# Kernel tuning notes

Measured on AMD Instinct MI355X. Metric: run time of the kernel, lower is better.

Reference implementation:

```python
import jax, jax.numpy as jnp
import numpy as np

NEG_INF = float('-inf')
B, T, C, U = 32, 1000, 500, 100
RISK_FACTOR = 0.1  # risk_strategy='exp', group_strategy='end'


def _lse3(x1, x2, x3):
    # numerically-safe logsumexp of 3 args, nan-free grads at -inf
    m = jnp.maximum(jnp.maximum(x1, x2), x3)
    dead = jnp.isneginf(m)
    ms = jnp.where(dead, 0.0, m)
    s = jnp.exp(x1 - ms) + jnp.exp(x2 - ms) + jnp.exp(x3 - ms)
    s = jnp.where(dead, 1.0, s)
    return jnp.where(dead, NEG_INF, ms + jnp.log(s))


def _safe_lse(x, axis):
    m = jnp.max(x, axis=axis, keepdims=True)
    dead = jnp.isneginf(m)
    ms = jnp.where(dead, 0.0, m)
    s = jnp.sum(jnp.exp(x - ms), axis=axis, keepdims=True)
    s = jnp.where(dead, 1.0, s)
    out = jnp.where(dead, NEG_INF, ms + jnp.log(s))
    return jnp.squeeze(out, axis)


def _log_sub_exp(a, b):
    # faithful port of espnet's log_substraction_exp: log(exp(a)-exp(b))
    mask1 = (~jnp.isinf(a)) & (~jnp.isinf(b))
    a_ = jnp.where(mask1, a, -1.0)
    b_ = jnp.where(mask1, b, -2.0)
    ans_tmp = b_ + jnp.log(jnp.exp(a_ - b_) - 1.0)
    a2 = jnp.where(jnp.isinf(ans_tmp), -2000.0, a_)
    b2 = jnp.where(jnp.isinf(ans_tmp), -2001.0, b_)
    ans1 = b2 + jnp.log(jnp.exp(a2 - b2) - 1.0)
    ans = jnp.where(mask1, ans1, jnp.full_like(a, NEG_INF))
    mask2 = (~jnp.isinf(a)) & jnp.isinf(b)
    return jnp.where(mask2, a, ans)


def _shift_r(x, n):
    return jnp.pad(x[:, :-n], ((0, 0), (n, 0)), constant_values=NEG_INF)


def _shift_l(x, n):
    return jnp.pad(x[:, n:], ((0, 0), (0, n)), constant_values=NEG_INF)


def _brctc_loss(nnet_output, ys_pad, hlens, ylens):
    # Dense equivalent of the k2 CTC lattice forward-backward in the log semiring.
    Bb, Tt, Cc = nnet_output.shape
    Uu = ys_pad.shape[1]
    S = 2 * Uu + 1  # extended label states: blank,y1,blank,...,yU,blank
    dt = nnet_output.dtype
    s_idx = jnp.arange(S)
    lab = ys_pad[:, jnp.clip((s_idx - 1) // 2, 0, Uu - 1)]        # [B,S]
    labels_ext = jnp.where((s_idx % 2 == 1)[None, :], lab, 0)
    prev_lab = ys_pad[:, jnp.clip((s_idx - 3) // 2, 0, Uu - 1)]
    allow_skip = ((s_idx % 2 == 1) & (s_idx >= 3))[None, :] & (lab != prev_lab)
    # p_ext[b,t,s] = nnet_output[b,t,labels_ext[b,s]]
    p_ext = jnp.take_along_axis(
        nnet_output, jnp.broadcast_to(labels_ext[:, None, :], (Bb, Tt, S)), axis=2)
    valid_s = s_idx[None, :] <= 2 * ylens[:, None]                # states beyond 2*ylen don't exist
    p_ext = jnp.where(valid_s[:, None, :], p_ext, NEG_INF)
    p_tbs = jnp.transpose(p_ext, (1, 0, 2))                       # [T,B,S]

    # forward: alpha[t,s] includes emission at frame t
    def fstep(a, pt):
        anew = pt + _lse3(a, _shift_r(a, 1),
                          jnp.where(allow_skip, _shift_r(a, 2), NEG_INF))
        return anew, anew
    a0 = jnp.full((Bb, S), NEG_INF, dt).at[:, 0].set(0.0)  # virtual start state
    _, alpha = jax.lax.scan(fstep, a0, p_tbs)                     # [T,B,S]

    # backward: beta[t,s] covers frames t+1..hlen-1 (excludes emission at t)
    t_arr = jnp.arange(Tt)
    fin = (s_idx[None, :] == 2 * ylens[:, None]) | (s_idx[None, :] == 2 * ylens[:, None] - 1)
    beta_fin = jnp.where(fin, 0.0, NEG_INF).astype(dt)
    allow_skip_n2 = jnp.pad(allow_skip[:, 2:], ((0, 0), (0, 2)), constant_values=False)
    p_next = jnp.concatenate([p_tbs[1:], jnp.full((1, Bb, S), NEG_INF, dt)], axis=0)

    def bstep(bcarry, inp):
        t, pn = inp
        q = pn + bcarry
        cand = _lse3(q, _shift_l(q, 1),
                     jnp.where(allow_skip_n2, _shift_l(q, 2), NEG_INF))
        bnew = jnp.where((t == hlens - 1)[:, None], beta_fin, cand)
        return bnew, bnew
    _, beta = jax.lax.scan(bstep, jnp.full((Bb, S), NEG_INF, dt),
                           (t_arr, p_next), reverse=True)         # [T,B,S]

    alpha = jnp.transpose(alpha, (1, 2, 0))                       # [B,S,T]
    beta = jnp.transpose(beta, (1, 2, 0))
    alpha = jnp.where((t_arr[None, :] < hlens[:, None])[:, None, :], alpha, NEG_INF)

    # keep only label (odd) states, as in alpha[:, 1::2]
    a_l = alpha[:, 1::2, :]
    b_l = beta[:, 1::2, :]
    p_l = jnp.transpose(p_ext, (0, 2, 1))[:, 1::2, :]
    dead = jnp.isneginf(a_l)  # states absent from the lattice
    b_l = jnp.where(dead, NEG_INF, b_l)
    p_l = jnp.where(dead, NEG_INF, p_l)

    # beta' removes the self-loop continuation -> posterior of label u ending at t
    beta_prime = _log_sub_exp(b_l[:, :, :-1], b_l[:, :, 1:] + p_l[:, :, 1:])
    beta_prime = jnp.concatenate([beta_prime, b_l[:, :, -1:]], axis=-1)
    loss_state = a_l + beta_prime                                 # [B,U,T]

    # risk_strategy == 'exp': risk = -risk_factor * t / hlen
    risk = -RISK_FACTOR * (t_arr[None, None, :].astype(dt) / hlens[:, None, None].astype(dt))
    loss_state = loss_state + risk

    loss_u = _safe_lse(loss_state, 2)                             # [B,U]
    mask = ~jnp.isneginf(loss_u)
    last = jnp.sum(mask.astype(jnp.int32), axis=1) - 1            # = ylen-1
    loss = jnp.take_along_axis(loss_u, last[:, None], axis=1)[:, 0]
    return -loss


def setup_inputs():
    key = jax.random.key(0)
    k1, k2, k3, k4 = jax.random.split(key, 4)
    nnet_output = jax.nn.log_softmax(
        jax.random.normal(k1, (B, T, C), dtype=jnp.float32), axis=-1)
    ys_pad = jax.random.randint(k2, (B, U), 1, C, dtype=jnp.int32)  # labels, 0 = blank excluded
    ylens = jax.random.randint(k3, (B,), 80, U + 1, dtype=jnp.int32)
    hlens = jax.random.randint(k4, (B,), 800, T + 1, dtype=jnp.int32)
    return {'nnet_output': nnet_output, 'ys_pad': ys_pad, 'hlens': hlens, 'ylens': ylens}


def reference(nnet_output, ys_pad, hlens, ylens):
    return _brctc_loss(nnet_output, ys_pad, hlens, ylens)
```

## Files before the change

### kernel.cpp

```cpp
#include <hip/hip_runtime.h>
#include <math.h>

#define T_DIM 1000
#define C_DIM 500
#define U_DIM 100
#define PAD   16
#define AROWS (T_DIM + 5)
#define NEGINF (-INFINITY)
#define LROW  128

__device__ __forceinline__ float lse2s(float a, float b) {
    float m = fmaxf(a, b), mn = fminf(a, b);
    float r = m + __logf(1.0f + __expf(mn - m));
    return fmaxf(r, NEGINF);
}
__device__ __forceinline__ float lse3s(float x1, float x2, float x3) {
    float m = fmaxf(fmaxf(x1, x2), x3);
    float r = m + __logf(__expf(x1 - m) + __expf(x2 - m) + __expf(x3 - m));
    return fmaxf(r, NEGINF);
}
__device__ __forceinline__ float lse3f(float x1, float x2, float x3) {
    float m = fmaxf(fmaxf(x1, x2), x3);
    if (m == NEGINF) return NEGINF;
    return m + __logf(__expf(x1 - m) + __expf(x2 - m) + __expf(x3 - m));
}

__device__ __forceinline__ float log_sub_expf(float a, float b) {
    bool ia = isinf(a), ib = isinf(b);
    if (!ia && !ib) {
        float ans = b + __logf(__expf(a - b) - 1.0f);
        if (isinf(ans)) ans = -2001.0f + __logf(__expf(1.0f) - 1.0f);
        return ans;
    }
    if (!ia && ib) return a;
    return NEGINF;
}

__device__ __forceinline__ float dpp_shr1(float x) {
    int r = __builtin_amdgcn_update_dpp(__float_as_int(NEGINF), __float_as_int(x),
                                        0x138, 0xF, 0xF, false);
    return __int_as_float(r);
}
__device__ __forceinline__ float dpp_shl1(float x) {
    int r = __builtin_amdgcn_update_dpp(__float_as_int(NEGINF), __float_as_int(x),
                                        0x130, 0xF, 0xF, false);
    return __int_as_float(r);
}

#define LSTEP(tt, RA, RB, RP)                                                \
    {                                                                        \
        float a_nx = (RA), br_nx = (RB), p_nx = (RP);                        \
        float bl   = (a_t  == NEGINF) ? NEGINF : braw_t;                     \
        float term = (a_nx == NEGINF) ? NEGINF : (br_nx + p_nx);             \
        float bp = log_sub_expf(bl, term);                                   \
        float x = a_t + bp - 0.1f * (float)(tt) * inv_hl;                    \
        if (x != NEGINF) {                                                   \
            float nm = fmaxf(m, x);                                          \
            ssum = ssum * __expf(m - nm) + __expf(x - nm);                   \
            m = nm;                                                          \
        }                                                                    \
        a_t = a_nx; braw_t = br_nx;                                          \
    }

__device__ __forceinline__ void gather_chunk(
    const float* __restrict__ nb, const int* __restrict__ shY, int yl,
    float* __restrict__ lds, float* __restrict__ ldsb,
    float* __restrict__ Pg ,
    int row0, int j)
{
#pragma unroll
    for (int k = 0; k < 17; ++k) {
        int i = j + k * 384;
        if (i < 6400) {
            int r = i >> 7, q = i & 127;
            if (q <= 100) {
                int row = row0 + r;
                int col = (q < 100) ? shY[q] : 0;
                float v = (row < T_DIM) ? nb[(size_t)row * C_DIM + col] : NEGINF;
                if (q < 100) {
                    lds[r * LROW + q] = (q < yl) ? v : NEGINF;
                    if (Pg) Pg[(size_t)r * U_DIM + q] = v;
                } else {
                    ldsb[r] = v;
                }
            }
        }
    }
}


#define FWP(j, pOv, gv)                                                      \
    {                                                                        \
        float Osh = dpp_shr1(O0);                                            \
        float nE = (mzE_lo + (gv)) + lse2s(E0, Osh);                         \
        float nO = (pOv) + lse3s(O0, E0, Osh + mskFlo);                      \
        float nOsh = dpp_shr1(nO);                                           \
        if (L == 50)                                                         \
            ((float2*)rlyF)[(tbk + (j)) & 63] = make_float2(nOsh, nE);       \
        E0 = nE; O0 = nO;                                                    \
        if (st) stA[(j) * U_DIM] = nO;                                       \
    }

#define FWC(j, pOv, gv, rv)                                                  \
    {                                                                        \
        float Esh = dpp_shr1(E0); Esh = (L == 0) ? (rv).y : Esh;             \
        float Osh = dpp_shr1(O0); Osh = (L == 0) ? (rv).x : Osh;             \
        float nE = (mzE_hi + (gv)) + lse2s(E0, O0);                          \
        float nO = (pOv) + lse3s(O0, Esh, Osh + mskFhi);                     \
        E0 = nE; O0 = nO;                                                    \
        if (st) stA[(j) * U_DIM] = nO;                                       \
    }

#define BWP(j, pOv, gv, FINF)                                                \
    {                                                                        \
        const int t_ = tbk - (j);                                            \
        float qE = (mzE_hi + (gv)) + BE;                                     \
        float qO = (pOv) + BO;                                               \
        if (L == 0) rlyB[(999 - t_) & 63] = qO;                              \
        float qOsh = dpp_shl1(qO);                                           \
        float nE = lse2s(qE, qOsh);                                          \
        float nO = lse3s(qO, qE, qOsh + mskBhi);                             \
        if (FINF) { const bool fin = (t_ == hl1);                            \
            BE = fin ? fE_hi : nE; BO = fin ? fO_hi : nO;                    \
        } else { BE = nE; BO = nO; }                                         \
        if (st) stB[-(int)((j) * U_DIM)] = BO;                               \
    }

#define BWC(j, pOv, gv, FINF, rq)                                            \
    {                                                                        \
        const int t_ = tbk - (j);                                            \
        float qE = (mzE_lo + (gv)) + BE;                                     \
        float qO = (pOv) + BO;                                               \
        qO = (L == 50) ? (rq) : qO;                                          \
        float qEsh = dpp_shl1(qE);                                           \
        float qOsh = dpp_shl1(qO);                                           \
        float nE = lse2s(qE, qO);                                            \
        float nO = lse3s(qO, qEsh, qOsh + mskBlo);                           \
        if (FINF) { const bool fin = (t_ == hl1);                            \
            BE = fin ? fE_lo : nE; BO = fin ? fO_lo : nO;                    \
        } else { BE = nE; BO = nO; }                                         \
        if (st) stB[-(int)((j) * U_DIM)] = BO;                               \
    }

#define BWP_BLOCK(FINF)                                                      \
    {                                                                        \
        const int tbk = tb2 + kk;                                            \
        float p0 = bb2[(kk-0)*LROW + 50 + L], p1 = bb2[(kk-1)*LROW + 50 + L],\
              p2 = bb2[(kk-2)*LROW + 50 + L], p3 = bb2[(kk-3)*LROW + 50 + L],\
              p4 = bb2[(kk-4)*LROW + 50 + L], p5 = bb2[(kk-5)*LROW + 50 + L],\
              p6 = bb2[(kk-6)*LROW + 50 + L], p7 = bb2[(kk-7)*LROW + 50 + L],\
              p8 = bb2[(kk-8)*LROW + 50 + L], p9 = bb2[(kk-9)*LROW + 50 + L];\
        float g0 = bp2[kk-0], g1 = bp2[kk-1], g2 = bp2[kk-2], g3 = bp2[kk-3],\
              g4 = bp2[kk-4], g5 = bp2[kk-5], g6 = bp2[kk-6], g7 = bp2[kk-7],\
              g8 = bp2[kk-8], g9 = bp2[kk-9];                                \
        BWP(0,p0,g0,FINF) BWP(1,p1,g1,FINF) BWP(2,p2,g2,FINF)                \
        BWP(3,p3,g3,FINF) BWP(4,p4,g4,FINF) BWP(5,p5,g5,FINF)                \
        BWP(6,p6,g6,FINF) BWP(7,p7,g7,FINF) BWP(8,p8,g8,FINF)                \
        BWP(9,p9,g9,FINF)                                                    \
        asm volatile("s_waitcnt lgkmcnt(0)" ::: "memory");                   \
        if (L == 0) *(volatile int*)&prgB = (999 - tbk) + 10;                \
        stB -= 10 * U_DIM;                                                   \
    }

#define BWC_BLOCK(FINF)                                                      \
    {                                                                        \
        const int tbk = tb2 + kk;                                            \
        const int kb = 999 - tbk;                                            \
        while (*(volatile int*)&prgB < kb + 10)                              \
            __builtin_amdgcn_s_sleep(1);                                     \
        asm volatile("" ::: "memory");                                       \
        float q0 = rlyB[(kb+0)&63], q1 = rlyB[(kb+1)&63],                    \
              q2 = rlyB[(kb+2)&63], q3 = rlyB[(kb+3)&63],                    \
              q4 = rlyB[(kb+4)&63], q5 = rlyB[(kb+5)&63],                    \
              q6 = rlyB[(kb+6)&63], q7 = rlyB[(kb+7)&63],                    \
              q8 = rlyB[(kb+8)&63], q9 = rlyB[(kb+9)&63];                    \
        float p0 = bb2[(kk-0)*LROW + L], p1 = bb2[(kk-1)*LROW + L],          \
              p2 = bb2[(kk-2)*LROW + L], p3 = bb2[(kk-3)*LROW + L],          \
              p4 = bb2[(kk-4)*LROW + L], p5 = bb2[(kk-5)*LROW + L],          \
              p6 = bb2[(kk-6)*LROW + L], p7 = bb2[(kk-7)*LROW + L],          \
              p8 = bb2[(kk-8)*LROW + L], p9 = bb2[(kk-9)*LROW + L];          \
        float g0 = bp2[kk-0], g1 = bp2[kk-1], g2 = bp2[kk-2], g3 = bp2[kk-3],\
              g4 = bp2[kk-4], g5 = bp2[kk-5], g6 = bp2[kk-6], g7 = bp2[kk-7],\
              g8 = bp2[kk-8], g9 = bp2[kk-9];                                \
        BWC(0,p0,g0,FINF,q0) BWC(1,p1,g1,FINF,q1) BWC(2,p2,g2,FINF,q2)       \
        BWC(3,p3,g3,FINF,q3) BWC(4,p4,g4,FINF,q4) BWC(5,p5,g5,FINF,q5)       \
        BWC(6,p6,g6,FINF,q6) BWC(7,p7,g7,FINF,q7) BWC(8,p8,g8,FINF,q8)       \
        BWC(9,p9,g9,FINF,q9)                                                 \
        stB -= 10 * U_DIM;                                                   \
    }

extern "C" __global__ void __launch_bounds__(1024)
brctc_fused(const float* __restrict__ nnet, const int* __restrict__ ys,
            const int* __restrict__ hlens, const int* __restrict__ ylens,
            float* __restrict__ P,
            float* __restrict__ A, float* __restrict__ Braw,
            float* __restrict__ out)
{
    const int b = blockIdx.x;
    const int tid = threadIdx.x;
    const int w = tid >> 6, L = tid & 63;
    const int hl = hlens[b], yl = ylens[b];
    const int hl1 = hl - 1;
    const size_t TP = T_DIM + 2 * PAD;
    const float* nb = nnet + (size_t)b * T_DIM * C_DIM;
    float* Pw = P + ((size_t)b * TP + PAD) * U_DIM;
    const float* Pb = Pw;
    const int* ysb = ys + b * U_DIM;
    float* Ab = A    + (size_t)b * AROWS * U_DIM;
    float* Bb = Braw + (size_t)b * AROWS * U_DIM;

    __shared__ __align__(16) float fbuf[2][50 * LROW];
    __shared__ __align__(16) float bbuf[2][50 * LROW];
    __shared__ float fpb[2][56], bpb[2][56];
    __shared__ float shm[8][U_DIM], shs[8][U_DIM], shlu[U_DIM];
    __shared__ int shY[U_DIM];
    __shared__ __align__(8) float rlyF[128];
    __shared__ float rlyB[64];
    __shared__ int prgF, prgB;

    if (tid < U_DIM) shY[tid] = ysb[tid];

    const int cl = U_DIM - 1;
    const int yL   = ysb[min(L, cl)];
    const int yLm1 = ysb[min(max(L - 1, 0), cl)];
    const int yLp1 = ysb[min(L + 1, cl)];
    const int y50L = ysb[min(50 + L, cl)];
    const int y49L = ysb[min(49 + L, cl)];
    const int y51L = ysb[min(51 + L, cl)];
    const int ty = 2 * yl;
    const bool st = (L < 50);
    const float mzE_lo = (L <= 50 && 2 * L <= ty)       ? 0.0f : NEGINF;
    const float mzE_hi = (L <= 49 && 102 + 2 * L <= ty) ? 0.0f : NEGINF;
    const float mskFlo = (L >= 1 && yL != yLm1)  ? 0.0f : NEGINF;
    const float mskFhi = (y50L != y49L)          ? 0.0f : NEGINF;
    const float mskBhi = (L <= 48 && y51L != y50L) ? 0.0f : NEGINF;
    const float mskBlo = (yLp1 != yL)            ? 0.0f : NEGINF;
    const float fE_lo = (2*L     == ty || 2*L     == ty-1) ? 0.0f : NEGINF;
    const float fO_lo = (2*L+1   == ty || 2*L+1   == ty-1) ? 0.0f : NEGINF;
    const float fE_hi = (102+2*L == ty || 102+2*L == ty-1) ? 0.0f : NEGINF;
    const float fO_hi = (101+2*L == ty || 101+2*L == ty-1) ? 0.0f : NEGINF;

    float E0, O0, BE, BO;
    E0 = (w == 0 && L == 0) ? 0.0f : NEGINF;
    O0 = NEGINF; BE = NEGINF; BO = NEGINF;

    __syncthreads();

    if (w == 0 && L == 0) {
        prgF = 0; prgB = 0;
        ((float2*)rlyF)[63] = make_float2(NEGINF, NEGINF);
    }
    if (w >= 4) {
        int j2 = tid - 256;
        for (int i = j2; i < 4 * 50 * 28; i += 768) {
            int buf = i / (50 * 28), rem = i % (50 * 28);
            int r = rem / 28, q = 100 + rem % 28;
            float* base = (buf == 0) ? fbuf[0] : (buf == 1) ? fbuf[1]
                        : (buf == 2) ? bbuf[0] : bbuf[1];
            base[r * LROW + q] = NEGINF;
        }
    }
    if (w >= 4 && w < 10) {
        int j = tid - 256;
        gather_chunk(nb, shY, yl, fbuf[0], fpb[0], Pw, 0, j);
        if (j < U_DIM) Pw[(size_t)T_DIM * U_DIM + j] = NEGINF;
    } else if (w >= 10) {
        int j = tid - 640;
        gather_chunk(nb, shY, yl, bbuf[0], bpb[0], nullptr, 951, j);
    }
    __syncthreads();

    for (int c = 0; c < 20; ++c) {
        if (w == 0) {
            const float* fb = fbuf[c & 1];
            const float* fp = fpb[c & 1];
            const int tb = 50 * c;
            float* stA = Ab + (size_t)tb * U_DIM + L;
            for (int kk = 0; kk < 50; kk += 10) {
                const int tbk = tb + kk;
                float p0 = fb[(kk+0)*LROW + L], p1 = fb[(kk+1)*LROW + L],
                      p2 = fb[(kk+2)*LROW + L], p3 = fb[(kk+3)*LROW + L],
                      p4 = fb[(kk+4)*LROW + L], p5 = fb[(kk+5)*LROW + L],
                      p6 = fb[(kk+6)*LROW + L], p7 = fb[(kk+7)*LROW + L],
                      p8 = fb[(kk+8)*LROW + L], p9 = fb[(kk+9)*LROW + L];
                float g0 = fp[kk+0], g1 = fp[kk+1], g2 = fp[kk+2],
                      g3 = fp[kk+3], g4 = fp[kk+4], g5 = fp[kk+5],
                      g6 = fp[kk+6], g7 = fp[kk+7], g8 = fp[kk+8],
                      g9 = fp[kk+9];
                FWP(0,p0,g0) FWP(1,p1,g1) FWP(2,p2,g2) FWP(3,p3,g3)
                FWP(4,p4,g4) FWP(5,p5,g5) FWP(6,p6,g6) FWP(7,p7,g7)
                FWP(8,p8,g8) FWP(9,p9,g9)
                asm volatile("s_waitcnt lgkmcnt(0)" ::: "memory");
                if (L == 0) *(volatile int*)&prgF = tbk + 10;
                stA += 10 * U_DIM;
            }
        } else if (w == 1) {
            const float* fb = fbuf[c & 1];
            const float* fp = fpb[c & 1];
            const int tb = 50 * c;
            float* stA = Ab + (size_t)tb * U_DIM + 50 + L;
            for (int kk = 0; kk < 50; kk += 10) {
                const int tbk = tb + kk;
                while (*(volatile int*)&prgF < tbk + 9)
                    __builtin_amdgcn_s_sleep(1);
                asm volatile("" ::: "memory");
                const float2* rf = (const float2*)rlyF;
                float2 v0 = rf[(tbk + 63) & 63], v1 = rf[(tbk + 0) & 63],
                       v2 = rf[(tbk + 1) & 63],  v3 = rf[(tbk + 2) & 63],
                       v4 = rf[(tbk + 3) & 63],  v5 = rf[(tbk + 4) & 63],
                       v6 = rf[(tbk + 5) & 63],  v7 = rf[(tbk + 6) & 63],
                       v8 = rf[(tbk + 7) & 63],  v9 = rf[(tbk + 8) & 63];
                float p0 = fb[(kk+0)*LROW + 50 + L], p1 = fb[(kk+1)*LROW + 50 + L],
                      p2 = fb[(kk+2)*LROW + 50 + L], p3 = fb[(kk+3)*LROW + 50 + L],
                      p4 = fb[(kk+4)*LROW + 50 + L], p5 = fb[(kk+5)*LROW + 50 + L],
                      p6 = fb[(kk+6)*LROW + 50 + L], p7 = fb[(kk+7)*LROW + 50 + L],
                      p8 = fb[(kk+8)*LROW + 50 + L], p9 = fb[(kk+9)*LROW + 50 + L];
                float g0 = fp[kk+0], g1 = fp[kk+1], g2 = fp[kk+2],
                      g3 = fp[kk+3], g4 = fp[kk+4], g5 = fp[kk+5],
                      g6 = fp[kk+6], g7 = fp[kk+7], g8 = fp[kk+8],
                      g9 = fp[kk+9];
                FWC(0,p0,g0,v0) FWC(1,p1,g1,v1) FWC(2,p2,g2,v2) FWC(3,p3,g3,v3)
                FWC(4,p4,g4,v4) FWC(5,p5,g5,v5) FWC(6,p6,g6,v6) FWC(7,p7,g7,v7)
                FWC(8,p8,g8,v8) FWC(9,p9,g9,v9)
                stA += 10 * U_DIM;
            }
        } else if (w == 2) {
            const float* bb2 = bbuf[c & 1];
            const float* bp2 = bpb[c & 1];
            const int cc = 19 - c;
            const int tb2 = 50 * cc;
            float* stB = Bb + (size_t)(tb2 + 49) * U_DIM + 50 + L;
            if (hl1 >= tb2 && hl1 <= tb2 + 49) {
                for (int kk = 49; kk >= 9; kk -= 10) BWP_BLOCK(true)
            } else {
                for (int kk = 49; kk >= 9; kk -= 10) BWP_BLOCK(false)
            }
        } else if (w == 3) {
            const float* bb2 = bbuf[c & 1];
            const float* bp2 = bpb[c & 1];
            const int cc = 19 - c;
            const int tb2 = 50 * cc;
            float* stB = Bb + (size_t)(tb2 + 49) * U_DIM + L;
            if (hl1 >= tb2 && hl1 <= tb2 + 49) {
                for (int kk = 49; kk >= 9; kk -= 10) BWC_BLOCK(true)
            } else {
                for (int kk = 49; kk >= 9; kk -= 10) BWC_BLOCK(false)
            }
        } else if (c < 19) {
            if (w < 10) {
                int j = tid - 256;
                int row0 = (c + 1) * 50;
                gather_chunk(nb, shY, yl, fbuf[(c + 1) & 1], fpb[(c + 1) & 1],
                             Pw + (size_t)row0 * U_DIM, row0, j);
            } else {
                int j = tid - 640;
                int row0 = (18 - c) * 50 + 1;
                gather_chunk(nb, shY, yl, bbuf[(c + 1) & 1], bpb[(c + 1) & 1],
                             nullptr, row0, j);
            }
        }
        __syncthreads();
    }

    if (w == 0 && st)
        ((float2*)(Ab + (size_t)T_DIM * U_DIM))[L] = make_float2(NEGINF, NEGINF);

    {
        const int r0f = min(hl, T_DIM);
        const int nrow = T_DIM + 1 - r0f;
        const int tot = nrow * 50;
        for (int i = tid; i < tot; i += 1024) {
            const int rr = r0f + i / 50, cc2 = i % 50;
            ((float2*)(Ab + (size_t)rr * U_DIM))[cc2] = make_float2(NEGINF, NEGINF);
        }
    }
    __syncthreads();

    {
        const int u = tid & 127;
        const int c = tid >> 7;
        if (u < U_DIM) {
            const bool valu = (u < yl);
            const float inv_hl = 1.0f / (float)hl;
            const int t0 = 125 * c;
            float a_t    = Ab[(size_t)t0 * U_DIM + u];
            float braw_t = Bb[(size_t)t0 * U_DIM + u];
            float aA0 = Ab[(long)(t0 + 1) * U_DIM + u];
            float aA1 = Ab[(long)(t0 + 2) * U_DIM + u];
            float aA2 = Ab[(long)(t0 + 3) * U_DIM + u];
            float aA3 = Ab[(long)(t0 + 4) * U_DIM + u];
            float bA0 = Bb[(long)(t0 + 1) * U_DIM + u];
            float bA1 = Bb[(long)(t0 + 2) * U_DIM + u];
            float bA2 = Bb[(long)(t0 + 3) * U_DIM + u];
            float bA3 = Bb[(long)(t0 + 4) * U_DIM + u];
            float pA0 = valu ? Pb[(long)(t0 + 1) * U_DIM + u] : NEGINF;
            float pA1 = valu ? Pb[(long)(t0 + 2) * U_DIM + u] : NEGINF;
            float pA2 = valu ? Pb[(long)(t0 + 3) * U_DIM + u] : NEGINF;
            float pA3 = valu ? Pb[(long)(t0 + 4) * U_DIM + u] : NEGINF;
            float m = NEGINF, ssum = 0.0f;
            for (int kb = 0; kb <= 120; kb += 4) {
                long nr = (long)(t0 + kb + 5);
                float aB0 = Ab[(nr + 0) * U_DIM + u];
                float aB1 = Ab[(nr + 1) * U_DIM + u];
                float aB2 = Ab[(nr + 2) * U_DIM + u];
                float aB3 = Ab[(nr + 3) * U_DIM + u];
                float bB0 = Bb[(nr + 0) * U_DIM + u];
                float bB1 = Bb[(nr + 1) * U_DIM + u];
                float bB2 = Bb[(nr + 2) * U_DIM + u];
                float bB3 = Bb[(nr + 3) * U_DIM + u];
                float pB0 = valu ? Pb[(nr + 0) * U_DIM + u] : NEGINF;
                float pB1 = valu ? Pb[(nr + 1) * U_DIM + u] : NEGINF;
                float pB2 = valu ? Pb[(nr + 2) * U_DIM + u] : NEGINF;
                float pB3 = valu ? Pb[(nr + 3) * U_DIM + u] : NEGINF;
                LSTEP(t0 + kb + 0, aA0, bA0, pA0)
                LSTEP(t0 + kb + 1, aA1, bA1, pA1)
                LSTEP(t0 + kb + 2, aA2, bA2, pA2)
                LSTEP(t0 + kb + 3, aA3, bA3, pA3)
                aA0 = aB0; aA1 = aB1; aA2 = aB2; aA3 = aB3;
                bA0 = bB0; bA1 = bB1; bA2 = bB2; bA3 = bB3;
                pA0 = pB0; pA1 = pB1; pA2 = pB2; pA3 = pB3;
            }
            LSTEP(t0 + 124, aA0, bA0, pA0)
            shm[c][u] = m; shs[c][u] = ssum;
        }
    }
    __syncthreads();
    if (tid < U_DIM) {
        float M = NEGINF;
#pragma unroll
        for (int c = 0; c < 8; ++c) M = fmaxf(M, shm[c][tid]);
        float lu = NEGINF;
        if (M != NEGINF) {
            float s = 0.0f;
#pragma unroll
            for (int c = 0; c < 8; ++c) {
                float mc = shm[c][tid];
                if (mc != NEGINF) s += shs[c][tid] * __expf(mc - M);
            }
            lu = M + __logf(s);
        }
        shlu[tid] = lu;
    }
    __syncthreads();
    if (tid == 0) {
        int cnt = 0;
        for (int u = 0; u < U_DIM; ++u) cnt += (shlu[u] != NEGINF) ? 1 : 0;
        int last = cnt - 1;
        last = last < 0 ? 0 : (last > U_DIM - 1 ? U_DIM - 1 : last);
        out[b] = -shlu[last];
    }
}

extern "C" __global__ void __launch_bounds__(256)
brctc_fwd_fb(const float* __restrict__ nnet, const int* __restrict__ ys,
             const int* __restrict__ hlens, const int* __restrict__ ylens,
             float* __restrict__ a_l)
{
    const int b = blockIdx.x;
    const int s = threadIdx.x;
    __shared__ float sh_a[201];
    __shared__ int   sh_ys[U_DIM];
    if (s < U_DIM) sh_ys[s] = ys[b * U_DIM + s];
    __syncthreads();
    const int hl = hlens[b], yl = ylens[b];
    int lab = 0; bool skip = false;
    if (s < 201) {
        if (s & 1) lab = sh_ys[(s - 1) >> 1];
        if ((s & 1) && s >= 3) skip = (sh_ys[(s - 1) >> 1] != sh_ys[(s - 3) >> 1]);
        sh_a[s] = (s == 0) ? 0.0f : NEGINF;
    }
    const bool valid = (s < 201) && (s <= 2 * yl);
    const bool isodd = (s < 201) && (s & 1);
    const int l = (s - 1) >> 1;
    const float* base = nnet + (size_t)b * T_DIM * C_DIM;
    float* alb = a_l + (size_t)b * T_DIM * U_DIM;
    __syncthreads();
    float p_cur = valid ? base[lab] : NEGINF;
    for (int t = 0; t < T_DIM; ++t) {
        float p_nxt = (valid && (t + 1 < T_DIM)) ? base[(size_t)(t + 1) * C_DIM + lab] : NEGINF;
        float x1 = (s < 201) ? sh_a[s] : NEGINF;
        float x2 = (s >= 1 && s < 201) ? sh_a[s - 1] : NEGINF;
        float x3 = skip ? sh_a[s - 2] : NEGINF;
        float anew = p_cur + lse3f(x1, x2, x3);
        __syncthreads();
        if (s < 201) sh_a[s] = anew;
        if (isodd) alb[t * U_DIM + l] = (t < hl) ? anew : NEGINF;
        __syncthreads();
        p_cur = p_nxt;
    }
}

extern "C" __global__ void __launch_bounds__(256)
brctc_bwd_fb(const float* __restrict__ nnet, const int* __restrict__ ys,
             const int* __restrict__ hlens, const int* __restrict__ ylens,
             const float* __restrict__ a_l, float* __restrict__ out)
{
    const int b = blockIdx.x;
    const int s = threadIdx.x;
    __shared__ float sh_b[201], sh_q[201], sh_lu[U_DIM];
    __shared__ int sh_ys[U_DIM];
    if (s < U_DIM) sh_ys[s] = ys[b * U_DIM + s];
    __syncthreads();
    const int hl = hlens[b], yl = ylens[b];
    int lab = 0; bool skip2 = false;
    if (s < 201) {
        if (s & 1) lab = sh_ys[(s - 1) >> 1];
        int s2 = s + 2;
        if (s2 < 201 && (s2 & 1) && s2 >= 3)
            skip2 = (sh_ys[(s2 - 1) >> 1] != sh_ys[(s2 - 3) >> 1]);
        sh_b[s] = NEGINF;
    }
    const bool valid = (s < 201) && (s <= 2 * yl);
    const bool isodd = (s < 201) && (s & 1);
    const int l = (s - 1) >> 1;
    const float fin0 = (s == 2 * yl || s == 2 * yl - 1) ? 0.0f : NEGINF;
    const float* base = nnet + (size_t)b * T_DIM * C_DIM;
    const float* alb = a_l + (size_t)b * T_DIM * U_DIM;
    float m_run = NEGINF, acc = 0.0f, prev_bl = NEGINF, p_hi = NEGINF;
    __syncthreads();
    for (int t = T_DIM - 1; t >= 0; --t) {
        float p_lo = valid ? base[(size_t)t * C_DIM + lab] : NEGINF;
        float a_cur = isodd ? alb[t * U_DIM + l] : NEGINF;
        float q = (s < 201) ? (p_hi + sh_b[s]) : NEGINF;
        if (s < 201) sh_q[s] = q;
        __syncthreads();
        float q2 = (s + 1 < 201) ? sh_q[s + 1] : NEGINF;
        float q3 = skip2 ? sh_q[s + 2] : NEGINF;
        float cand = lse3f(q, q2, q3);
        float bnew = (t == hl - 1) ? fin0 : cand;
        if (s < 201) sh_b[s] = bnew;
        if (isodd) {
            float bl_t = (a_cur == NEGINF) ? NEGINF : bnew;
            float bp = (t == T_DIM - 1) ? bl_t : log_sub_expf(bl_t, prev_bl + p_hi);
            float x = a_cur + bp - 0.1f * ((float)t / (float)hl);
            if (x != NEGINF) {
                if (x <= m_run) acc += __expf(x - m_run);
                else { acc = acc * __expf(m_run - x) + 1.0f; m_run = x; }
            }
            prev_bl = bl_t;
        }
        __syncthreads();
        p_hi = p_lo;
    }
    if (isodd) sh_lu[l] = (m_run == NEGINF) ? NEGINF : (m_run + __logf(acc));
    __syncthreads();
    if (s == 0) {
        int cnt = 0;
        for (int u = 0; u < U_DIM; ++u) cnt += (sh_lu[u] != NEGINF) ? 1 : 0;
        int last = cnt - 1;
        last = last < 0 ? 0 : (last > U_DIM - 1 ? U_DIM - 1 : last);
        out[b] = -sh_lu[last];
    }
}

extern "C" void kernel_launch(void* const* d_in, const int* in_sizes, int n_in,
                              void* d_out, int out_size, void* d_ws, size_t ws_size,
                              hipStream_t stream) {
    const float* nnet  = (const float*)d_in[0];
    const int*   ys    = (const int*)d_in[1];
    const int*   hlens = (const int*)d_in[2];
    const int*   ylens = (const int*)d_in[3];
    float*       outp  = (float*)d_out;
    const int B = in_sizes[2];
    const size_t TP = T_DIM + 2 * PAD;
    const size_t szP  = (size_t)B * TP * U_DIM;
    const size_t szA  = (size_t)B * AROWS * U_DIM;
    const size_t need = (szP + 2 * szA) * sizeof(float);

    if (ws_size >= need) {
        float* P    = (float*)d_ws;
        float* A    = P + szP;
        float* Braw = A + szA;
        brctc_fused<<<B, 1024, 0, stream>>>(nnet, ys, hlens, ylens, P, A, Braw, outp);
    } else {
        float* A = (float*)d_ws;
        brctc_fwd_fb<<<B, 256, 0, stream>>>(nnet, ys, hlens, ylens, A);
        brctc_bwd_fb<<<B, 256, 0, stream>>>(nnet, ys, hlens, ylens, A, outp);
    }
}
```

Baseline: 368.3 us.

## Replace spin-wait producer/consumer with chunk-skewed pipeline via triple buffering

The lower and upper halves of the forward and backward CTC recursions now run one chunk apart, separated by the block barrier, instead of the upper-half wave spin-waiting on a shared progress counter after every 10 steps. Chunk buffers go from double to triple buffering and the relay ring doubles to 128 entries, so a full 50-step chunk of boundary values survives until the consumer reads it. LROW shrinks to 120 so the extra buffers fit in LDS. The cost is one extra loop iteration of pipeline fill and drain, plus more shared memory.

New measurement: 345.5 us. -6.2%, faster.

```diff
diff --git a/kernel.cpp b/kernel.cpp
--- a/kernel.cpp
+++ b/kernel.cpp
@@ -7,7 +7,7 @@
 #define PAD   16
 #define AROWS (T_DIM + 5)
 #define NEGINF (-INFINITY)
-#define LROW  128
+#define LROW  120
 
 __device__ __forceinline__ float lse2s(float a, float b) {
     float m = fmaxf(a, b), mn = fminf(a, b);
@@ -96,7 +96,7 @@
         float nO = (pOv) + lse3s(O0, E0, Osh + mskFlo);                      \
         float nOsh = dpp_shr1(nO);                                           \
         if (L == 50)                                                         \
-            ((float2*)rlyF)[(tbk + (j)) & 63] = make_float2(nOsh, nE);       \
+            ((float2*)rlyF)[(tbk + (j)) & 127] = make_float2(nOsh, nE);      \
         E0 = nE; O0 = nO;                                                    \
         if (st) stA[(j) * U_DIM] = nO;                                       \
     }
@@ -116,7 +116,7 @@
         const int t_ = tbk - (j);                                            \
         float qE = (mzE_hi + (gv)) + BE;                                     \
         float qO = (pOv) + BO;                                               \
-        if (L == 0) rlyB[(999 - t_) & 63] = qO;                              \
+        if (L == 0) rlyB[(999 - t_) & 127] = qO;                             \
         float qOsh = dpp_shl1(qO);                                           \
         float nE = lse2s(qE, qOsh);                                          \
         float nO = lse3s(qO, qE, qOsh + mskBhi);                             \
@@ -157,8 +157,6 @@
         BWP(3,p3,g3,FINF) BWP(4,p4,g4,FINF) BWP(5,p5,g5,FINF)                \
         BWP(6,p6,g6,FINF) BWP(7,p7,g7,FINF) BWP(8,p8,g8,FINF)                \
         BWP(9,p9,g9,FINF)                                                    \
-        asm volatile("s_waitcnt lgkmcnt(0)" ::: "memory");                   \
-        if (L == 0) *(volatile int*)&prgB = (999 - tbk) + 10;                \
         stB -= 10 * U_DIM;                                                   \
     }
 
@@ -166,14 +164,11 @@
     {                                                                        \
         const int tbk = tb2 + kk;                                            \
         const int kb = 999 - tbk;                                            \
-        while (*(volatile int*)&prgB < kb + 10)                              \
-            __builtin_amdgcn_s_sleep(1);                                     \
-        asm volatile("" ::: "memory");                                       \
-        float q0 = rlyB[(kb+0)&63], q1 = rlyB[(kb+1)&63],                    \
-              q2 = rlyB[(kb+2)&63], q3 = rlyB[(kb+3)&63],                    \
-              q4 = rlyB[(kb+4)&63], q5 = rlyB[(kb+5)&63],                    \
-              q6 = rlyB[(kb+6)&63], q7 = rlyB[(kb+7)&63],                    \
-              q8 = rlyB[(kb+8)&63], q9 = rlyB[(kb+9)&63];                    \
+        float q0 = rlyB[(kb+0)&127], q1 = rlyB[(kb+1)&127],                  \
+              q2 = rlyB[(kb+2)&127], q3 = rlyB[(kb+3)&127],                  \
+              q4 = rlyB[(kb+4)&127], q5 = rlyB[(kb+5)&127],                  \
+              q6 = rlyB[(kb+6)&127], q7 = rlyB[(kb+7)&127],                  \
+              q8 = rlyB[(kb+8)&127], q9 = rlyB[(kb+9)&127];                  \
         float p0 = bb2[(kk-0)*LROW + L], p1 = bb2[(kk-1)*LROW + L],          \
               p2 = bb2[(kk-2)*LROW + L], p3 = bb2[(kk-3)*LROW + L],          \
               p4 = bb2[(kk-4)*LROW + L], p5 = bb2[(kk-5)*LROW + L],          \
@@ -209,14 +204,13 @@
     float* Ab = A    + (size_t)b * AROWS * U_DIM;
     float* Bb = Braw + (size_t)b * AROWS * U_DIM;
 
-    __shared__ __align__(16) float fbuf[2][50 * LROW];
-    __shared__ __align__(16) float bbuf[2][50 * LROW];
-    __shared__ float fpb[2][56], bpb[2][56];
+    __shared__ __align__(16) float fbuf[3][50 * LROW];
+    __shared__ __align__(16) float bbuf[3][50 * LROW];
+    __shared__ float fpb[3][56], bpb[3][56];
     __shared__ float shm[8][U_DIM], shs[8][U_DIM], shlu[U_DIM];
     __shared__ int shY[U_DIM];
-    __shared__ __align__(8) float rlyF[128];
-    __shared__ float rlyB[64];
-    __shared__ int prgF, prgB;
+    __shared__ __align__(8) float rlyF[256];
+    __shared__ float rlyB[128];
 
     if (tid < U_DIM) shY[tid] = ysb[tid];
 
@@ -246,17 +240,16 @@
 
     __syncthreads();
 
-    if (w == 0 && L == 0) {
-        prgF = 0; prgB = 0;
-        ((float2*)rlyF)[63] = make_float2(NEGINF, NEGINF);
-    }
+    if (w == 0 && L == 0)
+        ((float2*)rlyF)[127] = make_float2(NEGINF, NEGINF);
     if (w >= 4) {
         int j2 = tid - 256;
-        for (int i = j2; i < 4 * 50 * 28; i += 768) {
-            int buf = i / (50 * 28), rem = i % (50 * 28);
-            int r = rem / 28, q = 100 + rem % 28;
+        for (int i = j2; i < 6 * 50 * 20; i += 768) {
+            int buf = i / 1000, rem = i % 1000;
+            int r = rem / 20, q = 100 + rem % 20;
             float* base = (buf == 0) ? fbuf[0] : (buf == 1) ? fbuf[1]
-                        : (buf == 2) ? bbuf[0] : bbuf[1];
+                        : (buf == 2) ? fbuf[2] : (buf == 3) ? bbuf[0]
+                        : (buf == 4) ? bbuf[1] : bbuf[2];
             base[r * LROW + q] = NEGINF;
         }
     }
@@ -270,92 +263,98 @@
     }
     __syncthreads();
 
-    for (int c = 0; c < 20; ++c) {
+    for (int i = 0; i < 21; ++i) {
         if (w == 0) {
-            const float* fb = fbuf[c & 1];
-            const float* fp = fpb[c & 1];
-            const int tb = 50 * c;
-            float* stA = Ab + (size_t)tb * U_DIM + L;
-            for (int kk = 0; kk < 50; kk += 10) {
-                const int tbk = tb + kk;
-                float p0 = fb[(kk+0)*LROW + L], p1 = fb[(kk+1)*LROW + L],
-                      p2 = fb[(kk+2)*LROW + L], p3 = fb[(kk+3)*LROW + L],
-                      p4 = fb[(kk+4)*LROW + L], p5 = fb[(kk+5)*LROW + L],
-                      p6 = fb[(kk+6)*LROW + L], p7 = fb[(kk+7)*LROW + L],
-                      p8 = fb[(kk+8)*LROW + L], p9 = fb[(kk+9)*LROW + L];
-                float g0 = fp[kk+0], g1 = fp[kk+1], g2 = fp[kk+2],
-                      g3 = fp[kk+3], g4 = fp[kk+4], g5 = fp[kk+5],
-                      g6 = fp[kk+6], g7 = fp[kk+7], g8 = fp[kk+8],
-                      g9 = fp[kk+9];
-                FWP(0,p0,g0) FWP(1,p1,g1) FWP(2,p2,g2) FWP(3,p3,g3)
-                FWP(4,p4,g4) FWP(5,p5,g5) FWP(6,p6,g6) FWP(7,p7,g7)
-                FWP(8,p8,g8) FWP(9,p9,g9)
-                asm volatile("s_waitcnt lgkmcnt(0)" ::: "memory");
-                if (L == 0) *(volatile int*)&prgF = tbk + 10;
-                stA += 10 * U_DIM;
+            if (i < 20) {
+                const float* fb = fbuf[i % 3];
+                const float* fp = fpb[i % 3];
+                const int tb = 50 * i;
+                float* stA = Ab + (size_t)tb * U_DIM + L;
+                for (int kk = 0; kk < 50; kk += 10) {
+                    const int tbk = tb + kk;
+                    float p0 = fb[(kk+0)*LROW + L], p1 = fb[(kk+1)*LROW + L],
+                          p2 = fb[(kk+2)*LROW + L], p3 = fb[(kk+3)*LROW + L],
+                          p4 = fb[(kk+4)*LROW + L], p5 = fb[(kk+5)*LROW + L],
+                          p6 = fb[(kk+6)*LROW + L], p7 = fb[(kk+7)*LROW + L],
+                          p8 = fb[(kk+8)*LROW + L], p9 = fb[(kk+9)*LROW + L];
+                    float g0 = fp[kk+0], g1 = fp[kk+1], g2 = fp[kk+2],
+                          g3 = fp[kk+3], g4 = fp[kk+4], g5 = fp[kk+5],
+                          g6 = fp[kk+6], g7 = fp[kk+7], g8 = fp[kk+8],
+                          g9 = fp[kk+9];
+                    FWP(0,p0,g0) FWP(1,p1,g1) FWP(2,p2,g2) FWP(3,p3,g3)
+                    FWP(4,p4,g4) FWP(5,p5,g5) FWP(6,p6,g6) FWP(7,p7,g7)
+                    FWP(8,p8,g8) FWP(9,p9,g9)
+                    stA += 10 * U_DIM;
+                }
             }
         } else if (w == 1) {
-            const float* fb = fbuf[c & 1];
-            const float* fp = fpb[c & 1];
-            const int tb = 50 * c;
-            float* stA = Ab + (size_t)tb * U_DIM + 50 + L;
-            for (int kk = 0; kk < 50; kk += 10) {
-                const int tbk = tb + kk;
-                while (*(volatile int*)&prgF < tbk + 9)
-                    __builtin_amdgcn_s_sleep(1);
-                asm volatile("" ::: "memory");
-                const float2* rf = (const float2*)rlyF;
-                float2 v0 = rf[(tbk + 63) & 63], v1 = rf[(tbk + 0) & 63],
-                       v2 = rf[(tbk + 1) & 63],  v3 = rf[(tbk + 2) & 63],
-                       v4 = rf[(tbk + 3) & 63],  v5 = rf[(tbk + 4) & 63],
-                       v6 = rf[(tbk + 5) & 63],  v7 = rf[(tbk + 6) & 63],
-                       v8 = rf[(tbk + 7) & 63],  v9 = rf[(tbk + 8) & 63];
-                float p0 = fb[(kk+0)*LROW + 50 + L], p1 = fb[(kk+1)*LROW + 50 + L],
-                      p2 = fb[(kk+2)*LROW + 50 + L], p3 = fb[(kk+3)*LROW + 50 + L],
-                      p4 = fb[(kk+4)*LROW + 50 + L], p5 = fb[(kk+5)*LROW + 50 + L],
-                      p6 = fb[(kk+6)*LROW + 50 + L], p7 = fb[(kk+7)*LROW + 50 + L],
-                      p8 = fb[(kk+8)*LROW + 50 + L], p9 = fb[(kk+9)*LROW + 50 + L];
-                float g0 = fp[kk+0], g1 = fp[kk+1], g2 = fp[kk+2],
-                      g3 = fp[kk+3], g4 = fp[kk+4], g5 = fp[kk+5],
-                      g6 = fp[kk+6], g7 = fp[kk+7], g8 = fp[kk+8],
-                      g9 = fp[kk+9];
-                FWC(0,p0,g0,v0) FWC(1,p1,g1,v1) FWC(2,p2,g2,v2) FWC(3,p3,g3,v3)
-                FWC(4,p4,g4,v4) FWC(5,p5,g5,v5) FWC(6,p6,g6,v6) FWC(7,p7,g7,v7)
-                FWC(8,p8,g8,v8) FWC(9,p9,g9,v9)
-                stA += 10 * U_DIM;
+            if (i >= 1) {
+                const int ci = i - 1;
+                const float* fb = fbuf[ci % 3];
+                const float* fp = fpb[ci % 3];
+                const int tb = 50 * ci;
+                float* stA = Ab + (size_t)tb * U_DIM + 50 + L;
+                for (int kk = 0; kk < 50; kk += 10) {
+                    const int tbk = tb + kk;
+                    const float2* rf = (const float2*)rlyF;
+                    float2 v0 = rf[(tbk + 127) & 127], v1 = rf[(tbk + 0) & 127],
+                           v2 = rf[(tbk + 1) & 127],   v3 = rf[(tbk + 2) & 127],
+                           v4 = rf[(tbk + 3) & 127],   v5 = rf[(tbk + 4) & 127],
+                           v6 = rf[(tbk + 5) & 127],   v7 = rf[(tbk + 6) & 127],
+                           v8 = rf[(tbk + 7) & 127],   v9 = rf[(tbk + 8) & 127];
+                    float p0 = fb[(kk+0)*LROW + 50 + L], p1 = fb[(kk+1)*LROW + 50 + L],
+                          p2 = fb[(kk+2)*LROW + 50 + L], p3 = fb[(kk+3)*LROW + 50 + L],
+                          p4 = fb[(kk+4)*LROW + 50 + L], p5 = fb[(kk+5)*LROW + 50 + L],
+                          p6 = fb[(kk+6)*LROW + 50 + L], p7 = fb[(kk+7)*LROW + 50 + L],
+                          p8 = fb[(kk+8)*LROW + 50 + L], p9 = fb[(kk+9)*LROW + 50 + L];
+                    float g0 = fp[kk+0], g1 = fp[kk+1], g2 = fp[kk+2],
+                          g3 = fp[kk+3], g4 = fp[kk+4], g5 = fp[kk+5],
+                          g6 = fp[kk+6], g7 = fp[kk+7], g8 = fp[kk+8],
+                          g9 = fp[kk+9];
+                    FWC(0,p0,g0,v0) FWC(1,p1,g1,v1) FWC(2,p2,g2,v2) FWC(3,p3,g3,v3)
+                    FWC(4,p4,g4,v4) FWC(5,p5,g5,v5) FWC(6,p6,g6,v6) FWC(7,p7,g7,v7)
+                    FWC(8,p8,g8,v8) FWC(9,p9,g9,v9)
+                    stA += 10 * U_DIM;
+                }
             }
         } else if (w == 2) {
-            const float* bb2 = bbuf[c & 1];
-            const float* bp2 = bpb[c & 1];
-            const int cc = 19 - c;
-            const int tb2 = 50 * cc;
-            float* stB = Bb + (size_t)(tb2 + 49) * U_DIM + 50 + L;
-            if (hl1 >= tb2 && hl1 <= tb2 + 49) {
-                for (int kk = 49; kk >= 9; kk -= 10) BWP_BLOCK(true)
-            } else {
-                for (int kk = 49; kk >= 9; kk -= 10) BWP_BLOCK(false)
+            if (i < 20) {
+                const float* bb2 = bbuf[i % 3];
+                const float* bp2 = bpb[i % 3];
+                const int cc = 19 - i;
+                const int tb2 = 50 * cc;
+                float* stB = Bb + (size_t)(tb2 + 49) * U_DIM + 50 + L;
+                if (hl1 >= tb2 && hl1 <= tb2 + 49) {
+                    for (int kk = 49; kk >= 9; kk -= 10) BWP_BLOCK(true)
+                } else {
+                    for (int kk = 49; kk >= 9; kk -= 10) BWP_BLOCK(false)
+                }
             }
         } else if (w == 3) {
-            const float* bb2 = bbuf[c & 1];
-            const float* bp2 = bpb[c & 1];
-            const int cc = 19 - c;
-            const int tb2 = 50 * cc;
-            float* stB = Bb + (size_t)(tb2 + 49) * U_DIM + L;
-            if (hl1 >= tb2 && hl1 <= tb2 + 49) {
-                for (int kk = 49; kk >= 9; kk -= 10) BWC_BLOCK(true)
-            } else {
-                for (int kk = 49; kk >= 9; kk -= 10) BWC_BLOCK(false)
-            }
-        } else if (c < 19) {
+            if (i >= 1) {
+                const int ci = i - 1;
+                const float* bb2 = bbuf[ci % 3];
+                const float* bp2 = bpb[ci % 3];
+                const int cc = 19 - ci;
+                const int tb2 = 50 * cc;
+                float* stB = Bb + (size_t)(tb2 + 49) * U_DIM + L;
+                if (hl1 >= tb2 && hl1 <= tb2 + 49) {
+                    for (int kk = 49; kk >= 9; kk -= 10) BWC_BLOCK(true)
+                } else {
+                    for (int kk = 49; kk >= 9; kk -= 10) BWC_BLOCK(false)
+                }
+            }
+        } else if (i < 19) {
+            const int bi = (i + 1) % 3;
             if (w < 10) {
                 int j = tid - 256;
-                int row0 = (c + 1) * 50;
-                gather_chunk(nb, shY, yl, fbuf[(c + 1) & 1], fpb[(c + 1) & 1],
+                int row0 = (i + 1) * 50;
+                gather_chunk(nb, shY, yl, fbuf[bi], fpb[bi],
                              Pw + (size_t)row0 * U_DIM, row0, j);
             } else {
                 int j = tid - 640;
-                int row0 = (18 - c) * 50 + 1;
-                gather_chunk(nb, shY, yl, bbuf[(c + 1) & 1], bpb[(c + 1) & 1],
+                int row0 = (18 - i) * 50 + 1;
+                gather_chunk(nb, shY, yl, bbuf[bi], bpb[bi],
                              nullptr, row0, j);
             }
         }
```
